# Optimization experiments

Measured on AMD Instinct MI355X. Metric: run time of the kernel, lower is better.

Reference implementation:

```python
import jax, jax.numpy as jnp
import numpy as np

B, N, D, H = 4, 2048, 1024, 16
HD = D // H
SCALE = D ** -0.5  # NOTE: original scales by dimension**-0.5 (not head_dim**-0.5)


def setup_inputs() -> dict:
    key = jax.random.key(0)
    k1, k2, k3 = jax.random.split(key, 3)
    x = jax.random.normal(k1, (B, N, D), dtype=jnp.float32)
    w_qkv = jax.random.normal(k2, (D, 3 * D), dtype=jnp.float32) * (D ** -0.5)
    w_proj = jax.random.normal(k3, (D, D), dtype=jnp.float32) * (D ** -0.5)
    b_proj = jnp.zeros((D,), dtype=jnp.float32)
    return {"x": x, "w_qkv": w_qkv, "w_proj": w_proj, "b_proj": b_proj}


def reference(x, w_qkv, w_proj, b_proj):
    # qkv projection: [B,N,3D] -> split into q,k,v each [B,H,N,HD]
    qkv = x @ w_qkv
    qkv = qkv.reshape(B, N, 3, H, HD).transpose(2, 0, 3, 1, 4)  # [3,B,H,N,HD]
    q, k, v = qkv[0], qkv[1], qkv[2]
    scores = jnp.einsum('bhid,bhjd->bhij', q, k) * SCALE
    attn = jax.nn.softmax(scores, axis=-1)
    out = jnp.einsum('bhij,bhjd->bhid', attn, v)  # [B,H,N,HD]
    out = out.transpose(0, 2, 1, 3).reshape(B, N, D)
    return out @ w_proj + b_proj
```

## Files before the change

### kernel.cpp

```cpp
#include <hip/hip_runtime.h>
#include <stdint.h>

#define Bdim 4
#define Nseq 2048
#define Dmod 1024
#define Hn   16
#define HD   64
#define SCALE 0.03125f
#define L2E   1.44269504089f

typedef __attribute__((ext_vector_type(8))) short short8;
typedef __attribute__((ext_vector_type(8))) unsigned short ushort8;
typedef __attribute__((ext_vector_type(4))) float f32x4;
typedef __attribute__((ext_vector_type(16))) float f32x16;

typedef __attribute__((address_space(3))) uint32_t lds_u32;
typedef __attribute__((address_space(1))) const uint32_t glob_u32;

static __device__ __forceinline__ void gload_lds16(const unsigned short* g, unsigned short* l) {
    __builtin_amdgcn_global_load_lds((glob_u32*)(const void*)g, (lds_u32*)(void*)l, 16, 0, 0);
}

static __device__ __forceinline__ unsigned short f2bf(float f) {
    union { float f; uint32_t u; } v; v.f = f;
    uint32_t r = (v.u + 0x7FFFu + ((v.u >> 16) & 1u)) >> 16;
    return (unsigned short)r;
}

__global__ __launch_bounds__(256) void prep_kernel(const float* __restrict__ x,
                                                   const float* __restrict__ w_qkv,
                                                   const float* __restrict__ w_proj,
                                                   unsigned short* __restrict__ xb,
                                                   unsigned short* __restrict__ wqkvT,
                                                   unsigned short* __restrict__ wprojT) {
    __shared__ unsigned short t[32][33];
    int bid = blockIdx.x, tid = threadIdx.x;
    if (bid < 2048) {
        const int n4 = (Bdim * Nseq * Dmod) / 4;
        int i = bid * 256 + tid;
        for (; i < n4; i += 2048 * 256) {
            float4 v = reinterpret_cast<const float4*>(x)[i];
            ushort4 o;
            o.x = f2bf(v.x); o.y = f2bf(v.y); o.z = f2bf(v.z); o.w = f2bf(v.w);
            reinterpret_cast<ushort4*>(xb)[i] = o;
        }
        return;
    }
    const float* in;
    unsigned short* out;
    int R, C, c0, r0;
    if (bid < 5120) {
        int lin = bid - 2048;
        in = w_qkv; out = wqkvT; R = 1024; C = 3072;
        c0 = (lin % 96) * 32; r0 = (lin / 96) * 32;
    } else {
        int lin = bid - 5120;
        in = w_proj; out = wprojT; R = 1024; C = 1024;
        c0 = (lin % 32) * 32; r0 = (lin / 32) * 32;
    }
    int tx = tid & 31, ty = tid >> 5;
#pragma unroll
    for (int i = 0; i < 4; ++i)
        t[ty + i*8][tx] = f2bf(in[(size_t)(r0 + ty + i*8) * C + c0 + tx]);
    __syncthreads();
#pragma unroll
    for (int i = 0; i < 4; ++i)
        out[(size_t)(c0 + ty + i*8) * R + r0 + tx] = t[tx][ty + i*8];
}

template<bool OUT_BF16, bool BIAS, bool VSPLIT>
__global__ __launch_bounds__(512, 2) void gemm_big_kernel(const unsigned short* __restrict__ A,
                                                          const unsigned short* __restrict__ Bt,
                                                          void* __restrict__ Cv,
                                                          const float* __restrict__ bias,
                                                          unsigned short* __restrict__ vTp,
                                                          int N, int GX) {
    const int K = 1024;
    __shared__ unsigned short Abuf[2 * 16384];
    __shared__ unsigned short Bbuf[2 * 8192];

    int tid = threadIdx.x;
    int lane = tid & 63, w = tid >> 6;
    int lr = lane & 15, lg = lane >> 4;

    int lin = blockIdx.x;
    int cpx = gridDim.x >> 3;
    int nl = (lin & 7) * cpx + (lin >> 3);
    int m0 = (nl / GX) * 256, n0 = (nl % GX) * 128;

    int wr = (w >> 1) * 64, wc = (w & 1) * 64;
    int miA0 = (wr >> 4), miB0 = (wc >> 4);

    const unsigned short* aS[4];
    unsigned short* aD[4];
#pragma unroll
    for (int j = 0; j < 4; ++j) {
        int mi = w * 2 + (j >> 1), kk = j & 1;
        aS[j] = A + (size_t)(m0 + mi * 16 + lr) * K + kk * 32 + lg * 8;
        aD[j] = Abuf + (w * 4 + j) * 512;
    }
    const unsigned short* bS[2];
    unsigned short* bD[2];
#pragma unroll
    for (int j = 0; j < 2; ++j) {
        bS[j] = Bt + (size_t)(n0 + w * 16 + lr) * K + j * 32 + lg * 8;
        bD[j] = Bbuf + (w * 2 + j) * 512;
    }

    f32x4 acc[4][4];
#pragma unroll
    for (int i = 0; i < 4; ++i)
#pragma unroll
        for (int j = 0; j < 4; ++j) acc[i][j] = (f32x4)0.f;

#pragma unroll
    for (int j = 0; j < 4; ++j) gload_lds16(aS[j], aD[j]);
#pragma unroll
    for (int j = 0; j < 2; ++j) gload_lds16(bS[j], bD[j]);
    asm volatile("s_waitcnt vmcnt(0)" ::: "memory");
    __builtin_amdgcn_s_barrier();

    for (int t = 0; t < 16; ++t) {
        if (t < 15) {
            int bo = ((t + 1) & 1);
#pragma unroll
            for (int j = 0; j < 4; ++j) gload_lds16(aS[j] + (t + 1) * 64, aD[j] + bo * 16384);
#pragma unroll
            for (int j = 0; j < 2; ++j) gload_lds16(bS[j] + (t + 1) * 64, bD[j] + bo * 8192);
        }
        const char* Ab = (const char*)Abuf + (t & 1) * 32768;
        const char* Bb = (const char*)Bbuf + (t & 1) * 16384;
        short8 af[4][2], bf[4][2];
#pragma unroll
        for (int mi = 0; mi < 4; ++mi)
#pragma unroll
            for (int kk = 0; kk < 2; ++kk)
                af[mi][kk] = *reinterpret_cast<const short8*>(
                    Ab + ((miA0 + mi) * 2 + kk) * 1024 + lane * 16);
#pragma unroll
        for (int ni = 0; ni < 4; ++ni)
#pragma unroll
            for (int kk = 0; kk < 2; ++kk)
                bf[ni][kk] = *reinterpret_cast<const short8*>(
                    Bb + ((miB0 + ni) * 2 + kk) * 1024 + lane * 16);
        __builtin_amdgcn_s_setprio(1);
#pragma unroll
        for (int mi = 0; mi < 4; ++mi)
#pragma unroll
            for (int ni = 0; ni < 4; ++ni)
#pragma unroll
                for (int kk = 0; kk < 2; ++kk)
                    acc[mi][ni] = __builtin_amdgcn_mfma_f32_16x16x32_bf16(
                        af[mi][kk], bf[ni][kk], acc[mi][ni], 0, 0, 0);
        __builtin_amdgcn_s_setprio(0);
        asm volatile("s_waitcnt vmcnt(0)" ::: "memory");
        __builtin_amdgcn_s_barrier();
    }

#pragma unroll
    for (int mi = 0; mi < 4; ++mi) {
#pragma unroll
        for (int ni = 0; ni < 4; ++ni) {
            int r = m0 + wr + mi*16 + lg*4;
            int c = n0 + wc + ni*16 + lr;
            if (VSPLIT && c >= 2048) {
                int cc = c - 2048;
                int bh = ((r >> 11) << 4) + (cc >> 6);
                int d = cc & 63;
                ushort4 o4;
                o4.x = f2bf(acc[mi][ni][0]);
                o4.y = f2bf(acc[mi][ni][1]);
                o4.z = f2bf(acc[mi][ni][2]);
                o4.w = f2bf(acc[mi][ni][3]);
                *reinterpret_cast<ushort4*>(vTp + ((size_t)(bh * 64 + d) * 2048) + (r & 2047)) = o4;
            } else {
                float bv = BIAS ? bias[c] : 0.f;
#pragma unroll
                for (int i = 0; i < 4; ++i) {
                    float v = acc[mi][ni][i] + bv;
                    if (OUT_BF16)
                        reinterpret_cast<unsigned short*>(Cv)[(size_t)(r + i) * N + c] = f2bf(v);
                    else
                        reinterpret_cast<float*>(Cv)[(size_t)(r + i) * N + c] = v;
                }
            }
        }
    }
}

__global__ __launch_bounds__(256, 2) void attn_kernel(const unsigned short* __restrict__ qkv,
                                                      const unsigned short* __restrict__ vT,
                                                      unsigned short* __restrict__ attn_o) {
    __shared__ unsigned short Kl[2 * 64 * 64];
    __shared__ unsigned short Vl[2 * 64 * 64];
    __shared__ unsigned short Pl[4 * 64 * 64];

    int w = blockIdx.x;
    int lid = (w & 7) * 64 + (w >> 3);
    int bh = lid >> 3, qb = lid & 7;
    int b = bh >> 4, h = bh & 15;

    int tid = threadIdx.x, lane = tid & 63, wv = tid >> 6;
    int lr = lane & 31, hi = lane >> 5;
    int q0 = qb * 256 + wv * 64;

    short8 qfA[4], qfB[4];
    {
        const unsigned short* qrowA = qkv + (size_t)(b * Nseq + q0 + lr) * 3072 + h * 64 + hi * 8;
        const unsigned short* qrowB = qrowA + (size_t)32 * 3072;
#pragma unroll
        for (int ks = 0; ks < 4; ++ks) {
            qfA[ks] = *reinterpret_cast<const short8*>(qrowA + ks * 16);
            qfB[ks] = *reinterpret_cast<const short8*>(qrowB + ks * 16);
        }
    }

    float mrunA = -1e30f, lrunA = 0.f, mrunB = -1e30f, lrunB = 0.f;
    f32x16 oA0 = (f32x16)0.f, oA1 = (f32x16)0.f, oB0 = (f32x16)0.f, oB1 = (f32x16)0.f;

    int sr = tid >> 2;
    const unsigned short* kg = qkv + (size_t)(b * Nseq + sr) * 3072 + 1024 + h * 64 + (tid & 3) * 16;
    const unsigned short* vg = vT + ((size_t)(bh * 64 + sr)) * Nseq + (tid & 3) * 16;
    int sb = (sr >> 5) * 4096 + (tid & 3) * 1024 + (sr & 31) * 16;
    char* Pw = (char*)Pl + wv * 8192 + lr * 16 + 8 * hi;
    char* Pr = (char*)Pl + wv * 8192 + lane * 16;

    {
        ushort8 a0 = *reinterpret_cast<const ushort8*>(kg);
        ushort8 a1 = *reinterpret_cast<const ushort8*>(kg + 8);
        ushort8 a2 = *reinterpret_cast<const ushort8*>(vg);
        ushort8 a3 = *reinterpret_cast<const ushort8*>(vg + 8);
        *reinterpret_cast<ushort8*>((char*)Kl + sb) = a0;
        *reinterpret_cast<ushort8*>((char*)Kl + sb + 512) = a1;
        *reinterpret_cast<ushort8*>((char*)Vl + sb) = a2;
        *reinterpret_cast<ushort8*>((char*)Vl + sb + 512) = a3;
    }
    ushort8 k0r = *reinterpret_cast<const ushort8*>(kg + (size_t)64 * 3072);
    ushort8 k1r = *reinterpret_cast<const ushort8*>(kg + (size_t)64 * 3072 + 8);
    ushort8 v0r = *reinterpret_cast<const ushort8*>(vg + 64);
    ushort8 v1r = *reinterpret_cast<const ushort8*>(vg + 72);

    int cur = 0;
    for (int jt = 0; jt < Nseq; jt += 64, cur ^= 1) {
        __syncthreads();
        int rb = cur * 8192, wb = rb ^ 8192;

        f32x16 sA0 = (f32x16)0.f, sA1 = (f32x16)0.f, sB0 = (f32x16)0.f, sB1 = (f32x16)0.f;
        __builtin_amdgcn_s_setprio(1);
#pragma unroll
        for (int ks = 0; ks < 4; ++ks) {
            short8 kf0 = *reinterpret_cast<const short8*>((char*)Kl + rb + ks*1024 + lane*16);
            short8 kf1 = *reinterpret_cast<const short8*>((char*)Kl + rb + 4096 + ks*1024 + lane*16);
            sA0 = __builtin_amdgcn_mfma_f32_32x32x16_bf16(kf0, qfA[ks], sA0, 0, 0, 0);
            sA1 = __builtin_amdgcn_mfma_f32_32x32x16_bf16(kf1, qfA[ks], sA1, 0, 0, 0);
            sB0 = __builtin_amdgcn_mfma_f32_32x32x16_bf16(kf0, qfB[ks], sB0, 0, 0, 0);
            sB1 = __builtin_amdgcn_mfma_f32_32x32x16_bf16(kf1, qfB[ks], sB1, 0, 0, 0);
        }
        __builtin_amdgcn_s_setprio(0);

        if (jt + 64 < Nseq) {
            *reinterpret_cast<ushort8*>((char*)Kl + wb + sb) = k0r;
            *reinterpret_cast<ushort8*>((char*)Kl + wb + sb + 512) = k1r;
            *reinterpret_cast<ushort8*>((char*)Vl + wb + sb) = v0r;
            *reinterpret_cast<ushort8*>((char*)Vl + wb + sb + 512) = v1r;
            int jn = jt + 128;
            if (jn < Nseq) {
                k0r = *reinterpret_cast<const ushort8*>(kg + (size_t)jn * 3072);
                k1r = *reinterpret_cast<const ushort8*>(kg + (size_t)jn * 3072 + 8);
                v0r = *reinterpret_cast<const ushort8*>(vg + jn);
                v1r = *reinterpret_cast<const ushort8*>(vg + jn + 8);
            }
        }

        float tA[16], tB[16];
#pragma unroll
        for (int i = 0; i < 16; ++i) { tA[i] = fmaxf(sA0[i], sA1[i]); tB[i] = fmaxf(sB0[i], sB1[i]); }
#pragma unroll
        for (int st = 8; st > 0; st >>= 1)
#pragma unroll
            for (int i = 0; i < st; ++i) { tA[i] = fmaxf(tA[i], tA[i + st]); tB[i] = fmaxf(tB[i], tB[i + st]); }
        float mlocA = fmaxf(tA[0], __shfl_xor(tA[0], 32)) * SCALE;
        float mlocB = fmaxf(tB[0], __shfl_xor(tB[0], 32)) * SCALE;

        if (!__all((mlocA <= mrunA + 8.f) && (mlocB <= mrunB + 8.f))) {
            float mnA = fmaxf(mrunA, mlocA);
            float fA = __builtin_amdgcn_exp2f((mrunA - mnA) * L2E);
            float mnB = fmaxf(mrunB, mlocB);
            float fB = __builtin_amdgcn_exp2f((mrunB - mnB) * L2E);
            lrunA *= fA; lrunB *= fB; mrunA = mnA; mrunB = mnB;
#pragma unroll
            for (int i = 0; i < 16; ++i) {
                oA0[i] *= fA; oA1[i] *= fA; oB0[i] *= fB; oB1[i] *= fB;
            }
        }

        const float c1 = SCALE * L2E;
        float c0A = -mrunA * L2E, c0B = -mrunB * L2E;
        float pA0[16], pA1[16], pB0[16], pB1[16];
#pragma unroll
        for (int i = 0; i < 16; ++i) {
            pA0[i] = __builtin_amdgcn_exp2f(fmaf(sA0[i], c1, c0A));
            pA1[i] = __builtin_amdgcn_exp2f(fmaf(sA1[i], c1, c0A));
            pB0[i] = __builtin_amdgcn_exp2f(fmaf(sB0[i], c1, c0B));
            pB1[i] = __builtin_amdgcn_exp2f(fmaf(sB1[i], c1, c0B));
        }

        uint32_t WA[16], WB[16];
#pragma unroll
        for (int m = 0; m < 8; ++m) {
            asm("v_cvt_pk_bf16_f32 %0, %1, %2" : "=v"(WA[m])   : "v"(pA0[2*m]), "v"(pA0[2*m+1]));
            asm("v_cvt_pk_bf16_f32 %0, %1, %2" : "=v"(WA[8+m]) : "v"(pA1[2*m]), "v"(pA1[2*m+1]));
            asm("v_cvt_pk_bf16_f32 %0, %1, %2" : "=v"(WB[m])   : "v"(pB0[2*m]), "v"(pB0[2*m+1]));
            asm("v_cvt_pk_bf16_f32 %0, %1, %2" : "=v"(WB[8+m]) : "v"(pB1[2*m]), "v"(pB1[2*m+1]));
        }
#pragma unroll
        for (int tt = 0; tt < 8; ++tt) {
            uint64_t valA = (uint64_t)WA[2*tt] | ((uint64_t)WA[2*tt+1] << 32);
            uint64_t valB = (uint64_t)WB[2*tt] | ((uint64_t)WB[2*tt+1] << 32);
            char* pa = Pw + (tt >> 1) * 1024 + (tt & 1) * 512;
            *reinterpret_cast<uint64_t*>(pa) = valA;
            *reinterpret_cast<uint64_t*>(pa + 4096) = valB;
        }

        float aA[16], aB[16];
#pragma unroll
        for (int i = 0; i < 16; ++i) { aA[i] = pA0[i] + pA1[i]; aB[i] = pB0[i] + pB1[i]; }
#pragma unroll
        for (int st = 8; st > 0; st >>= 1)
#pragma unroll
            for (int i = 0; i < st; ++i) { aA[i] += aA[i + st]; aB[i] += aB[i + st]; }
        lrunA += aA[0] + __shfl_xor(aA[0], 32);
        lrunB += aB[0] + __shfl_xor(aB[0], 32);

        __builtin_amdgcn_s_setprio(1);
#pragma unroll
        for (int ks4 = 0; ks4 < 4; ++ks4) {
            short8 vf0 = *reinterpret_cast<const short8*>((char*)Vl + rb + ks4*1024 + lane*16);
            short8 vf1 = *reinterpret_cast<const short8*>((char*)Vl + rb + 4096 + ks4*1024 + lane*16);
            short8 pfA = *reinterpret_cast<const short8*>(Pr + ks4*1024);
            short8 pfB = *reinterpret_cast<const short8*>(Pr + 4096 + ks4*1024);
            oA0 = __builtin_amdgcn_mfma_f32_32x32x16_bf16(vf0, pfA, oA0, 0, 0, 0);
            oA1 = __builtin_amdgcn_mfma_f32_32x32x16_bf16(vf1, pfA, oA1, 0, 0, 0);
            oB0 = __builtin_amdgcn_mfma_f32_32x32x16_bf16(vf0, pfB, oB0, 0, 0, 0);
            oB1 = __builtin_amdgcn_mfma_f32_32x32x16_bf16(vf1, pfB, oB1, 0, 0, 0);
        }
        __builtin_amdgcn_s_setprio(0);
    }

    float invA = 1.f / lrunA, invB = 1.f / lrunB;
    unsigned short* orowA = attn_o + (size_t)(b * Nseq + q0 + lr) * Dmod + h * 64;
    unsigned short* orowB = attn_o + (size_t)(b * Nseq + q0 + 32 + lr) * Dmod + h * 64;
#pragma unroll
    for (int db = 0; db < 2; ++db)
#pragma unroll
        for (int g = 0; g < 4; ++g) {
            int d = db * 32 + 8 * g + 4 * hi;
            ushort4 o4;
            o4.x = f2bf((db ? oA1[4*g+0] : oA0[4*g+0]) * invA);
            o4.y = f2bf((db ? oA1[4*g+1] : oA0[4*g+1]) * invA);
            o4.z = f2bf((db ? oA1[4*g+2] : oA0[4*g+2]) * invA);
            o4.w = f2bf((db ? oA1[4*g+3] : oA0[4*g+3]) * invA);
            *reinterpret_cast<ushort4*>(orowA + d) = o4;
            o4.x = f2bf((db ? oB1[4*g+0] : oB0[4*g+0]) * invB);
            o4.y = f2bf((db ? oB1[4*g+1] : oB0[4*g+1]) * invB);
            o4.z = f2bf((db ? oB1[4*g+2] : oB0[4*g+2]) * invB);
            o4.w = f2bf((db ? oB1[4*g+3] : oB0[4*g+3]) * invB);
            *reinterpret_cast<ushort4*>(orowB + d) = o4;
        }
}

extern "C" void kernel_launch(void* const* d_in, const int* in_sizes, int n_in,
                              void* d_out, int out_size, void* d_ws, size_t ws_size,
                              hipStream_t stream) {
    const float* x      = (const float*)d_in[0];
    const float* w_qkv  = (const float*)d_in[1];
    const float* w_proj = (const float*)d_in[2];
    const float* b_proj = (const float*)d_in[3];
    float* out = (float*)d_out;
    char* ws = (char*)d_ws;

    unsigned short* qkv    = (unsigned short*)(ws);
    unsigned short* vT     = (unsigned short*)(ws + 50331648);
    unsigned short* xb     = (unsigned short*)(ws + 67108864);
    unsigned short* attn_o = xb;
    unsigned short* wqkvT  = (unsigned short*)(ws + 83886080);
    unsigned short* wprojT = (unsigned short*)(ws + 90177536);

    prep_kernel<<<6144, 256, 0, stream>>>(x, w_qkv, w_proj, xb, wqkvT, wprojT);
    gemm_big_kernel<true, false, true><<<768, 512, 0, stream>>>(
        xb, wqkvT, qkv, nullptr, vT, 3072, 24);
    attn_kernel<<<512, 256, 0, stream>>>(qkv, vT, attn_o);
    gemm_big_kernel<false, true, false><<<256, 512, 0, stream>>>(
        attn_o, wprojT, out, b_proj, nullptr, 1024, 8);
}
```

Baseline: 250.9 us.

## Use 256x256 GEMM tiles with an interleaved 4-stage LDS ring pipeline

Replaces the 256x128 double-buffered GEMM with a 256x256 tile per block (8 waves, each computing 128x64) and a ring of LDS stages. Global-to-LDS loads for the next k-tile are issued in halves between MFMA phases, using partial vmcnt waits so loads overlap compute. The aim is higher arithmetic intensity per block and better latency hiding. In exchange, occupancy drops to one block per CU, there are more barriers per iteration, and the grids shrink to 384 and 128 blocks, which may underfill the GPU, especially for the output projection.

```diff
diff --git a/kernel.cpp b/kernel.cpp
--- a/kernel.cpp
+++ b/kernel.cpp
@@ -69,15 +69,15 @@
 }
 
 template<bool OUT_BF16, bool BIAS, bool VSPLIT>
-__global__ __launch_bounds__(512, 2) void gemm_big_kernel(const unsigned short* __restrict__ A,
-                                                          const unsigned short* __restrict__ Bt,
-                                                          void* __restrict__ Cv,
-                                                          const float* __restrict__ bias,
-                                                          unsigned short* __restrict__ vTp,
-                                                          int N, int GX) {
+__global__ __launch_bounds__(512, 1) void gemm8p_kernel(const unsigned short* __restrict__ A,
+                                                        const unsigned short* __restrict__ Bt,
+                                                        void* __restrict__ Cv,
+                                                        const float* __restrict__ bias,
+                                                        unsigned short* __restrict__ vTp,
+                                                        int N, int GX) {
     const int K = 1024;
-    __shared__ unsigned short Abuf[2 * 16384];
-    __shared__ unsigned short Bbuf[2 * 8192];
+    __shared__ unsigned short Aring[4 * 8192];
+    __shared__ unsigned short Bring[4 * 8192];
 
     int tid = threadIdx.x;
     int lane = tid & 63, w = tid >> 6;
@@ -86,79 +86,123 @@
     int lin = blockIdx.x;
     int cpx = gridDim.x >> 3;
     int nl = (lin & 7) * cpx + (lin >> 3);
-    int m0 = (nl / GX) * 256, n0 = (nl % GX) * 128;
-
-    int wr = (w >> 1) * 64, wc = (w & 1) * 64;
-    int miA0 = (wr >> 4), miB0 = (wc >> 4);
-
-    const unsigned short* aS[4];
-    unsigned short* aD[4];
-#pragma unroll
-    for (int j = 0; j < 4; ++j) {
-        int mi = w * 2 + (j >> 1), kk = j & 1;
-        aS[j] = A + (size_t)(m0 + mi * 16 + lr) * K + kk * 32 + lg * 8;
-        aD[j] = Abuf + (w * 4 + j) * 512;
-    }
-    const unsigned short* bS[2];
-    unsigned short* bD[2];
-#pragma unroll
-    for (int j = 0; j < 2; ++j) {
-        bS[j] = Bt + (size_t)(n0 + w * 16 + lr) * K + j * 32 + lg * 8;
-        bD[j] = Bbuf + (w * 2 + j) * 512;
-    }
-
-    f32x4 acc[4][4];
-#pragma unroll
-    for (int i = 0; i < 4; ++i)
+    int m0 = (nl / GX) * 256, n0 = (nl % GX) * 256;
+
+    int miG0 = (w >> 2) * 8;
+    int niG0 = (w & 3) * 4;
+
+    const unsigned short* aS0 = A  + (size_t)(m0 + w * 16 + lr) * K + lg * 8;
+    const unsigned short* aS1 = aS0 + (size_t)128 * K;
+    const unsigned short* bS0 = Bt + (size_t)(n0 + w * 16 + lr) * K + lg * 8;
+    const unsigned short* bS1 = bS0 + (size_t)128 * K;
+    unsigned short* aD0 = Aring + w * 512;
+    unsigned short* aD1 = Aring + (8 + w) * 512;
+    unsigned short* bD0 = Bring + w * 512;
+    unsigned short* bD1 = Bring + (8 + w) * 512;
+
+    f32x4 acc[8][4];
+#pragma unroll
+    for (int i = 0; i < 8; ++i)
 #pragma unroll
         for (int j = 0; j < 4; ++j) acc[i][j] = (f32x4)0.f;
 
-#pragma unroll
-    for (int j = 0; j < 4; ++j) gload_lds16(aS[j], aD[j]);
-#pragma unroll
-    for (int j = 0; j < 2; ++j) gload_lds16(bS[j], bD[j]);
-    asm volatile("s_waitcnt vmcnt(0)" ::: "memory");
-    __builtin_amdgcn_s_barrier();
+    gload_lds16(aS0, aD0);             gload_lds16(aS1, aD1);
+    gload_lds16(bS0, bD0);             gload_lds16(bS1, bD1);
+    gload_lds16(aS0 + 32, aD0 + 8192); gload_lds16(aS1 + 32, aD1 + 8192);
+    gload_lds16(bS0 + 32, bD0 + 8192); gload_lds16(bS1 + 32, bD1 + 8192);
 
     for (int t = 0; t < 16; ++t) {
+        int sR = (t & 1) * 2;
+        int sW = sR ^ 2;
+        const char* A0p = (const char*)(Aring + sR * 8192);
+        const char* B0p = (const char*)(Bring + sR * 8192);
+        const char* A1p = A0p + 16384;
+        const char* B1p = B0p + 16384;
+        size_t ko = (size_t)(t + 1) * 64;
+        short8 a[4], b[4];
+
         if (t < 15) {
-            int bo = ((t + 1) & 1);
-#pragma unroll
-            for (int j = 0; j < 4; ++j) gload_lds16(aS[j] + (t + 1) * 64, aD[j] + bo * 16384);
-#pragma unroll
-            for (int j = 0; j < 2; ++j) gload_lds16(bS[j] + (t + 1) * 64, bD[j] + bo * 8192);
-        }
-        const char* Ab = (const char*)Abuf + (t & 1) * 32768;
-        const char* Bb = (const char*)Bbuf + (t & 1) * 16384;
-        short8 af[4][2], bf[4][2];
-#pragma unroll
-        for (int mi = 0; mi < 4; ++mi)
-#pragma unroll
-            for (int kk = 0; kk < 2; ++kk)
-                af[mi][kk] = *reinterpret_cast<const short8*>(
-                    Ab + ((miA0 + mi) * 2 + kk) * 1024 + lane * 16);
+            gload_lds16(aS0 + ko, aD0 + sW * 8192);
+            gload_lds16(aS1 + ko, aD1 + sW * 8192);
+            asm volatile("s_waitcnt vmcnt(6)" ::: "memory");
+        } else {
+            asm volatile("s_waitcnt vmcnt(4)" ::: "memory");
+        }
+        __builtin_amdgcn_s_barrier();
 #pragma unroll
         for (int ni = 0; ni < 4; ++ni)
-#pragma unroll
-            for (int kk = 0; kk < 2; ++kk)
-                bf[ni][kk] = *reinterpret_cast<const short8*>(
-                    Bb + ((miB0 + ni) * 2 + kk) * 1024 + lane * 16);
+            b[ni] = *reinterpret_cast<const short8*>(B0p + (niG0 + ni) * 1024 + lane * 16);
+#pragma unroll
+        for (int mi = 0; mi < 4; ++mi)
+            a[mi] = *reinterpret_cast<const short8*>(A0p + (miG0 + mi) * 1024 + lane * 16);
         __builtin_amdgcn_s_setprio(1);
 #pragma unroll
         for (int mi = 0; mi < 4; ++mi)
 #pragma unroll
             for (int ni = 0; ni < 4; ++ni)
-#pragma unroll
-                for (int kk = 0; kk < 2; ++kk)
-                    acc[mi][ni] = __builtin_amdgcn_mfma_f32_16x16x32_bf16(
-                        af[mi][kk], bf[ni][kk], acc[mi][ni], 0, 0, 0);
-        __builtin_amdgcn_s_setprio(0);
-        asm volatile("s_waitcnt vmcnt(0)" ::: "memory");
-        __builtin_amdgcn_s_barrier();
-    }
-
-#pragma unroll
-    for (int mi = 0; mi < 4; ++mi) {
+                acc[mi][ni] = __builtin_amdgcn_mfma_f32_16x16x32_bf16(a[mi], b[ni], acc[mi][ni], 0, 0, 0);
+        __builtin_amdgcn_s_setprio(0);
+        __builtin_amdgcn_s_barrier();
+
+        if (t < 15) {
+            gload_lds16(bS0 + ko, bD0 + sW * 8192);
+            gload_lds16(bS1 + ko, bD1 + sW * 8192);
+        }
+#pragma unroll
+        for (int mi = 0; mi < 4; ++mi)
+            a[mi] = *reinterpret_cast<const short8*>(A0p + (miG0 + 4 + mi) * 1024 + lane * 16);
+        __builtin_amdgcn_s_setprio(1);
+#pragma unroll
+        for (int mi = 0; mi < 4; ++mi)
+#pragma unroll
+            for (int ni = 0; ni < 4; ++ni)
+                acc[4 + mi][ni] = __builtin_amdgcn_mfma_f32_16x16x32_bf16(a[mi], b[ni], acc[4 + mi][ni], 0, 0, 0);
+        __builtin_amdgcn_s_setprio(0);
+        __builtin_amdgcn_s_barrier();
+
+        if (t < 15) {
+            gload_lds16(aS0 + ko + 32, aD0 + sW * 8192 + 8192);
+            gload_lds16(aS1 + ko + 32, aD1 + sW * 8192 + 8192);
+            asm volatile("s_waitcnt vmcnt(6)" ::: "memory");
+        } else {
+            asm volatile("s_waitcnt vmcnt(0)" ::: "memory");
+        }
+        __builtin_amdgcn_s_barrier();
+#pragma unroll
+        for (int ni = 0; ni < 4; ++ni)
+            b[ni] = *reinterpret_cast<const short8*>(B1p + (niG0 + ni) * 1024 + lane * 16);
+#pragma unroll
+        for (int mi = 0; mi < 4; ++mi)
+            a[mi] = *reinterpret_cast<const short8*>(A1p + (miG0 + mi) * 1024 + lane * 16);
+        __builtin_amdgcn_s_setprio(1);
+#pragma unroll
+        for (int mi = 0; mi < 4; ++mi)
+#pragma unroll
+            for (int ni = 0; ni < 4; ++ni)
+                acc[mi][ni] = __builtin_amdgcn_mfma_f32_16x16x32_bf16(a[mi], b[ni], acc[mi][ni], 0, 0, 0);
+        __builtin_amdgcn_s_setprio(0);
+        __builtin_amdgcn_s_barrier();
+
+        if (t < 15) {
+            gload_lds16(bS0 + ko + 32, bD0 + sW * 8192 + 8192);
+            gload_lds16(bS1 + ko + 32, bD1 + sW * 8192 + 8192);
+        }
+#pragma unroll
+        for (int mi = 0; mi < 4; ++mi)
+            a[mi] = *reinterpret_cast<const short8*>(A1p + (miG0 + 4 + mi) * 1024 + lane * 16);
+        __builtin_amdgcn_s_setprio(1);
+#pragma unroll
+        for (int mi = 0; mi < 4; ++mi)
+#pragma unroll
+            for (int ni = 0; ni < 4; ++ni)
+                acc[4 + mi][ni] = __builtin_amdgcn_mfma_f32_16x16x32_bf16(a[mi], b[ni], acc[4 + mi][ni], 0, 0, 0);
+        __builtin_amdgcn_s_setprio(0);
+        __builtin_amdgcn_s_barrier();
+    }
+
+    int wr = (w >> 2) * 128, wc = (w & 3) * 64;
+#pragma unroll
+    for (int mi = 0; mi < 8; ++mi) {
 #pragma unroll
         for (int ni = 0; ni < 4; ++ni) {
             int r = m0 + wr + mi*16 + lg*4;
@@ -387,9 +431,9 @@
     unsigned short* wprojT = (unsigned short*)(ws + 90177536);
 
     prep_kernel<<<6144, 256, 0, stream>>>(x, w_qkv, w_proj, xb, wqkvT, wprojT);
-    gemm_big_kernel<true, false, true><<<768, 512, 0, stream>>>(
-        xb, wqkvT, qkv, nullptr, vT, 3072, 24);
+    gemm8p_kernel<true, false, true><<<384, 512, 0, stream>>>(
+        xb, wqkvT, qkv, nullptr, vT, 3072, 12);
     attn_kernel<<<512, 256, 0, stream>>>(qkv, vT, attn_o);
-    gemm_big_kernel<false, true, false><<<256, 512, 0, stream>>>(
-        attn_o, wprojT, out, b_proj, nullptr, 1024, 8);
-}
+    gemm8p_kernel<false, true, false><<<128, 512, 0, stream>>>(
+        attn_o, wprojT, out, b_proj, nullptr, 1024, 4);
+}
```

Measured after the change: 257.4 us. 1.03x slower.
